# Kernel tuning notes

Measured on AMD Instinct MI355X. Metric: run time of the kernel, lower is better.

## Reference

```python
import jax, jax.numpy as jnp
import numpy as np

D = 1024
NUM_HEADS = 16
HEAD_DIM = D // NUM_HEADS
INIT_VALUES = 1e-4


def setup_inputs() -> dict:
    key = jax.random.key(0)
    ks = jax.random.split(key, 24)
    s = 0.02
    inp = {
        "v": jax.random.normal(ks[0], (8, 2048, D), dtype=jnp.float32),
        "l": jax.random.normal(ks[1], (8, 512, D), dtype=jnp.float32),
        "ln_v_g": jnp.ones((D,), jnp.float32),
        "ln_v_b": jnp.zeros((D,), jnp.float32),
        "ln_l_g": jnp.ones((D,), jnp.float32),
        "ln_l_b": jnp.zeros((D,), jnp.float32),
        "gamma_v": jnp.full((D,), INIT_VALUES, jnp.float32),
        "gamma_l": jnp.full((D,), INIT_VALUES, jnp.float32),
    }
    names = ["Wq_v2l", "Wk_v2l", "Wv_v2l", "Wo_v2l", "Wq_l2v", "Wk_l2v", "Wv_l2v", "Wo_l2v"]
    for i, n in enumerate(names):
        inp[n] = jax.random.normal(ks[2 + i], (D, D), dtype=jnp.float32) * s
        inp[n.replace("W", "b")] = jnp.zeros((D,), jnp.float32)
    return inp


def layer_norm(x, g, b, eps=1e-5):
    mu = jnp.mean(x, axis=-1, keepdims=True)
    var = jnp.var(x, axis=-1, keepdims=True)
    return (x - mu) * jax.lax.rsqrt(var + eps) * g + b


def mha(q_in, k_in, v_in, Wq, bq, Wk, bk, Wv, bv, Wo, bo):
    B, Sq, _ = q_in.shape
    Sk = k_in.shape[1]
    # torch Linear: x @ W.T + b
    q = (q_in @ Wq.T + bq).reshape(B, Sq, NUM_HEADS, HEAD_DIM)
    k = (k_in @ Wk.T + bk).reshape(B, Sk, NUM_HEADS, HEAD_DIM)
    v = (v_in @ Wv.T + bv).reshape(B, Sk, NUM_HEADS, HEAD_DIM)
    scores = jnp.einsum("bqhd,bkhd->bhqk", q, k) / np.sqrt(HEAD_DIM).astype(np.float32)
    attn = jax.nn.softmax(scores, axis=-1)
    ctx = jnp.einsum("bhqk,bkhd->bqhd", attn, v).reshape(B, Sq, D)
    return ctx @ Wo.T + bo


def reference(v, l, ln_v_g, ln_v_b, ln_l_g, ln_l_b, gamma_v, gamma_l,
              Wq_v2l, bq_v2l, Wk_v2l, bk_v2l, Wv_v2l, bv_v2l, Wo_v2l, bo_v2l,
              Wq_l2v, bq_l2v, Wk_l2v, bk_l2v, Wv_l2v, bv_l2v, Wo_l2v, bo_l2v):
    # eval mode: dropout and drop_path are identity
    v_norm = layer_norm(v, ln_v_g, ln_v_b)
    l_norm = layer_norm(l, ln_l_g, ln_l_b)
    updated_v = mha(v_norm, l_norm, l_norm,
                    Wq_v2l, bq_v2l, Wk_v2l, bk_v2l, Wv_v2l, bv_v2l, Wo_v2l, bo_v2l)
    updated_l = mha(l_norm, v_norm, v_norm,
                    Wq_l2v, bq_l2v, Wk_l2v, bk_l2v, Wv_l2v, bv_l2v, Wo_l2v, bo_l2v)
    v_out = v + gamma_v * updated_v
    l_out = l + gamma_l * updated_l
    return (v_out, l_out)
```

## Files before the change

kernel.cpp:

```cpp
#include <hip/hip_runtime.h>
#include <hip/hip_bf16.h>
#include <stdint.h>

typedef __bf16 bf16x8 __attribute__((ext_vector_type(8)));
typedef float f32x4 __attribute__((ext_vector_type(4)));
typedef float f32x16 __attribute__((ext_vector_type(16)));
typedef uint32_t u32x4 __attribute__((ext_vector_type(4)));
typedef unsigned short u16;

typedef __attribute__((address_space(1))) void as1_void;
typedef __attribute__((address_space(3))) void as3_void;

#define BAR() __builtin_amdgcn_s_barrier()
#define VMCNT(n) asm volatile("s_waitcnt vmcnt(" #n ")" ::: "memory")
#define LGKM0() asm volatile("s_waitcnt lgkmcnt(0)" ::: "memory")

__device__ __forceinline__ u16 f2bf(float f) {
  uint32_t u = __float_as_uint(f);
  u += 0x7fffu + ((u >> 16) & 1u);
  return (u16)(u >> 16);
}

struct Seg {
  const u16* W;
  const float* bias;
  u16* outb;
  float* outf;
  const float* res;
  const float* gamma;
  int mode;
  int sk;
  float ascale;
};

__global__ __launch_bounds__(256) void cvt8_kernel(
    const float4* s0, const float4* s1, const float4* s2, const float4* s3,
    const float4* s4, const float4* s5, const float4* s6, const float4* s7,
    ushort4* d0, ushort4* d1, ushort4* d2, ushort4* d3,
    ushort4* d4, ushort4* d5, ushort4* d6, ushort4* d7) {
  const float4* s; ushort4* d;
  switch (blockIdx.y) {
    case 0: s = s0; d = d0; break;
    case 1: s = s1; d = d1; break;
    case 2: s = s2; d = d2; break;
    case 3: s = s3; d = d3; break;
    case 4: s = s4; d = d4; break;
    case 5: s = s5; d = d5; break;
    case 6: s = s6; d = d6; break;
    default: s = s7; d = d7; break;
  }
  int i = blockIdx.x * 256 + threadIdx.x;
  float4 v = s[i];
  ushort4 o;
  o.x = f2bf(v.x); o.y = f2bf(v.y); o.z = f2bf(v.z); o.w = f2bf(v.w);
  d[i] = o;
}

__global__ __launch_bounds__(256) void ln_kernel(const float* __restrict__ x,
                                                 const float* __restrict__ g,
                                                 const float* __restrict__ b,
                                                 u16* __restrict__ out) {
  int row = blockIdx.x;
  int t = threadIdx.x;
  const float4* xr = (const float4*)(x + (size_t)row * 1024);
  float4 v = xr[t];
  float s = v.x + v.y + v.z + v.w;
  float s2 = v.x * v.x + v.y * v.y + v.z * v.z + v.w * v.w;
#pragma unroll
  for (int off = 1; off < 64; off <<= 1) {
    s += __shfl_xor(s, off);
    s2 += __shfl_xor(s2, off);
  }
  __shared__ float red[8];
  int wv = t >> 6;
  if ((t & 63) == 0) { red[wv] = s; red[4 + wv] = s2; }
  __syncthreads();
  s = red[0] + red[1] + red[2] + red[3];
  s2 = red[4] + red[5] + red[6] + red[7];
  float mu = s * (1.0f / 1024.0f);
  float var = s2 * (1.0f / 1024.0f) - mu * mu;
  float rstd = rsqrtf(var + 1e-5f);
  const float4 gv = ((const float4*)g)[t];
  const float4 bv = ((const float4*)b)[t];
  ushort4 o;
  o.x = f2bf((v.x - mu) * rstd * gv.x + bv.x);
  o.y = f2bf((v.y - mu) * rstd * gv.y + bv.y);
  o.z = f2bf((v.z - mu) * rstd * gv.z + bv.z);
  o.w = f2bf((v.w - mu) * rstd * gv.w + bv.w);
  ((ushort4*)out)[(size_t)row * 256 + t] = o;
}

__global__ __launch_bounds__(256, 3) void gemm_v8(
    const u16* __restrict__ A0, Seg s00, Seg s01, Seg s02, int mt0c, int nt0c,
    const u16* __restrict__ A1, Seg s10, Seg s11, Seg s12, int mt1c, int nt1c) {
  const int K = 1024;
  int bid = blockIdx.x;
  int nb0 = mt0c * nt0c;
  const u16* A;
  Seg sa, sb, sc;
  int mtiles, ntiles, lbid;
  if (bid < nb0) {
    A = A0; mtiles = mt0c; ntiles = nt0c; lbid = bid; sa = s00; sb = s01; sc = s02;
  } else {
    A = A1; mtiles = mt1c; ntiles = nt1c; lbid = bid - nb0; sa = s10; sb = s11; sc = s12;
  }
  int xcd = lbid & 7, q = lbid >> 3;
  int mchunk = mtiles >> 3;
  int mt = xcd * mchunk + q / ntiles;
  int nt = q % ntiles;
  int m0 = mt * 128;
  int si = nt >> 3;
  Seg seg = (si == 0) ? sa : (si == 1) ? sb : sc;
  int nl0 = (nt & 7) * 128;

  int t = threadIdx.x, lane = t & 63, wv = t >> 6;
  int wr = wv >> 1, wc = wv & 1;
  int lr = lane & 15, lg = lane >> 4;

  __shared__ u16 SA[3][128 * 32];
  __shared__ u16 SB[3][128 * 32];

  int row0 = t >> 2, c0 = t & 3;
  int sco = (c0 ^ ((row0 >> 1) & 3)) * 8;
  const u16* gA0 = A + (size_t)(m0 + row0) * K + sco;
  const u16* gB0 = seg.W + (size_t)(nl0 + row0) * K + sco;

  auto STAGE = [&](int slot, int kt) {
    __builtin_amdgcn_global_load_lds((const as1_void*)(gA0 + kt * 32),
                                     (as3_void*)(&SA[slot][0] + t * 8), 16, 0, 0);
    __builtin_amdgcn_global_load_lds((const as1_void*)(gA0 + (size_t)64 * K + kt * 32),
                                     (as3_void*)(&SA[slot][0] + 2048 + t * 8), 16, 0, 0);
    __builtin_amdgcn_global_load_lds((const as1_void*)(gB0 + kt * 32),
                                     (as3_void*)(&SB[slot][0] + t * 8), 16, 0, 0);
    __builtin_amdgcn_global_load_lds((const as1_void*)(gB0 + (size_t)64 * K + kt * 32),
                                     (as3_void*)(&SB[slot][0] + 2048 + t * 8), 16, 0, 0);
  };

  f32x4 acc[4][4] = {};

  STAGE(0, 0); STAGE(1, 1); STAGE(2, 2);
  VMCNT(8);
  BAR();

  int slot = 0;
  const int NKT = K / 32;
#pragma unroll 1
  for (int kt = 0; kt < NKT; ++kt) {
    bf16x8 aX[4], bX[4];
#pragma unroll
    for (int m = 0; m < 4; ++m) {
      int row = wr * 64 + m * 16 + lr;
      aX[m] = *(const bf16x8*)(&SA[slot][0] + row * 32 + ((lg ^ ((row >> 1) & 3)) * 8));
    }
#pragma unroll
    for (int n = 0; n < 4; ++n) {
      int row = wc * 64 + n * 16 + lr;
      bX[n] = *(const bf16x8*)(&SB[slot][0] + row * 32 + ((lg ^ ((row >> 1) & 3)) * 8));
    }
    __builtin_amdgcn_s_setprio(1);
#pragma unroll
    for (int m = 0; m < 4; ++m)
#pragma unroll
      for (int n = 0; n < 4; ++n)
        acc[m][n] = __builtin_amdgcn_mfma_f32_16x16x32_bf16(aX[m], bX[n], acc[m][n], 0, 0, 0);
    __builtin_amdgcn_s_setprio(0);
    LGKM0();
    if (kt + 2 < NKT) { VMCNT(4); }
    else if (kt + 1 < NKT) { VMCNT(0); }
    BAR();
    if (kt + 3 < NKT) STAGE(slot, kt + 3);
    slot = (slot == 2) ? 0 : slot + 1;
  }

  int rowb = m0 + wr * 64 + (lane >> 4) * 4;
#pragma unroll
  for (int m = 0; m < 4; ++m) {
#pragma unroll
    for (int n = 0; n < 4; ++n) {
      int scol = nl0 + wc * 64 + n * 16 + lr;
      float bcol = seg.bias[scol];
      int row = rowb + m * 16;
      if (seg.mode == 2) {
        int bb = row >> seg.sk;
        int ss = row & ((1 << seg.sk) - 1);
        int h = scol >> 6, d = scol & 63;
        ushort4 o;
        o.x = f2bf(acc[m][n][0] + bcol);
        o.y = f2bf(acc[m][n][1] + bcol);
        o.z = f2bf(acc[m][n][2] + bcol);
        o.w = f2bf(acc[m][n][3] + bcol);
        *(ushort4*)(seg.outb + ((((size_t)bb * 16 + h) * 64 + d) << seg.sk) + ss) = o;
      } else if (seg.mode == 0) {
#pragma unroll
        for (int r = 0; r < 4; ++r)
          seg.outb[(size_t)(row + r) * 1024 + scol] = f2bf((acc[m][n][r] + bcol) * seg.ascale);
      } else {
#pragma unroll
        for (int r = 0; r < 4; ++r) {
          size_t idx = (size_t)(row + r) * 1024 + scol;
          seg.outf[idx] = seg.res[idx] + seg.gamma[scol] * (acc[m][n][r] + bcol);
        }
      }
    }
  }
}

__global__ __launch_bounds__(256, 4) void attn2_kernel(
    const u16* __restrict__ Q0, const u16* __restrict__ K0,
    const u16* __restrict__ V0, u16* __restrict__ C0, int Sq0, int Sk0, int nqs0, int nb0,
    const u16* __restrict__ Q1, const u16* __restrict__ K1,
    const u16* __restrict__ V1, u16* __restrict__ C1, int Sq1, int Sk1, int nqs1) {
  int bid = blockIdx.x;
  const u16 *Q, *Kmat, *Vt;
  u16* ctx;
  int Sq, Sk, nq_shift, f;
  if (bid < nb0) {
    Q = Q0; Kmat = K0; Vt = V0; ctx = C0; Sq = Sq0; Sk = Sk0; nq_shift = nqs0; f = bid;
  } else {
    Q = Q1; Kmat = K1; Vt = V1; ctx = C1; Sq = Sq1; Sk = Sk1; nq_shift = nqs1; f = bid - nb0;
  }
  int xcd = f & 7, slot = f >> 3;
  int group = xcd * 16 + (slot >> nq_shift);
  int qt = slot & ((1 << nq_shift) - 1);
  int b = group >> 4, h = group & 15;
  int t = threadIdx.x, lane = t & 63, wv = t >> 6;
  int l31 = lane & 31, hi = lane >> 5;

  __shared__ u16 Ks[2][64 * 64];
  __shared__ u16 Vs[2][64 * 64];

  int q0 = qt * 128 + wv * 32;
  const u16* Qb = Q + (size_t)(b * Sq + q0 + l31) * 1024 + h * 64 + hi * 8;
  bf16x8 qf[4];
#pragma unroll
  for (int ds = 0; ds < 4; ++ds) qf[ds] = *(const bf16x8*)(Qb + ds * 16);

  int trow = t >> 3, tc = t & 7;
  int sc = (tc ^ (trow & 7)) * 8;
  const u16* gk = Kmat + (size_t)(b * Sk + trow) * 1024 + h * 64 + sc;
  const u16* gv = Vt + (size_t)((b * 16 + h) * 64 + trow) * Sk + sc;

  auto STAGE = [&](int buf, int kt) {
    const u16* k0 = gk + (size_t)(kt * 64) * 1024;
    const u16* v0 = gv + kt * 64;
    __builtin_amdgcn_global_load_lds((const as1_void*)k0, (as3_void*)(Ks[buf] + t * 8), 16, 0, 0);
    __builtin_amdgcn_global_load_lds((const as1_void*)(k0 + (size_t)32 * 1024), (as3_void*)(Ks[buf] + 2048 + t * 8), 16, 0, 0);
    __builtin_amdgcn_global_load_lds((const as1_void*)v0, (as3_void*)(Vs[buf] + t * 8), 16, 0, 0);
    __builtin_amdgcn_global_load_lds((const as1_void*)(v0 + (size_t)32 * Sk), (as3_void*)(Vs[buf] + 2048 + t * 8), 16, 0, 0);
  };

  STAGE(0, 0);
  __syncthreads();

  f32x16 acc0 = {}, acc1 = {};
  float m_run = -1e30f, l_run = 0.f;
  int sw = l31 & 7;

  int nt = Sk >> 6;
  for (int kt = 0; kt < nt; ++kt) {
    int cur = kt & 1;
    if (kt + 1 < nt) STAGE(cur ^ 1, kt + 1);
    const u16* kb = Ks[cur];
    f32x16 s0v = {}, s1v = {};
    __builtin_amdgcn_s_setprio(1);
#pragma unroll
    for (int ds = 0; ds < 4; ++ds) {
      int blk = 2 * ds + hi;
      bf16x8 ka0 = *(const bf16x8*)(kb + l31 * 64 + ((blk ^ sw) * 8));
      bf16x8 ka1 = *(const bf16x8*)(kb + (32 + l31) * 64 + ((blk ^ sw) * 8));
      s0v = __builtin_amdgcn_mfma_f32_32x32x16_bf16(ka0, qf[ds], s0v, 0, 0, 0);
      s1v = __builtin_amdgcn_mfma_f32_32x32x16_bf16(ka1, qf[ds], s1v, 0, 0, 0);
    }
    __builtin_amdgcn_s_setprio(0);
    float mx = s0v[0];
#pragma unroll
    for (int i = 1; i < 16; ++i) mx = fmaxf(mx, s0v[i]);
#pragma unroll
    for (int i = 0; i < 16; ++i) mx = fmaxf(mx, s1v[i]);
    mx = fmaxf(mx, __shfl_xor(mx, 32));
    if (__any(mx > m_run + 8.f)) {
      float mnew = fmaxf(m_run, mx);
      float fac = __builtin_amdgcn_exp2f(m_run - mnew);
#pragma unroll
      for (int r = 0; r < 16; ++r) {
        int src = (r & 3) + 8 * (r >> 2) + 4 * hi;
        float fr = __shfl(fac, src);
        acc0[r] *= fr;
        acc1[r] *= fr;
      }
      l_run *= fac;
      m_run = mnew;
    }
    float sum = 0.f;
#pragma unroll
    for (int i = 0; i < 16; ++i) {
      s0v[i] = __builtin_amdgcn_exp2f(s0v[i] - m_run);
      sum += s0v[i];
    }
#pragma unroll
    for (int i = 0; i < 16; ++i) {
      s1v[i] = __builtin_amdgcn_exp2f(s1v[i] - m_run);
      sum += s1v[i];
    }
    sum += __shfl_xor(sum, 32);
    l_run += sum;
    bf16x8 pa[4];
#pragma unroll
    for (int g = 0; g < 2; ++g) {
      const f32x16& s = g ? s1v : s0v;
#pragma unroll
      for (int half = 0; half < 2; ++half) {
        int o = half * 8;
        uint32_t a0, a1, b0, b1;
        asm("v_cvt_pk_bf16_f32 %0, %1, %2" : "=v"(a0) : "v"(s[o + 0]), "v"(s[o + 1]));
        asm("v_cvt_pk_bf16_f32 %0, %1, %2" : "=v"(a1) : "v"(s[o + 2]), "v"(s[o + 3]));
        asm("v_cvt_pk_bf16_f32 %0, %1, %2" : "=v"(b0) : "v"(s[o + 4]), "v"(s[o + 5]));
        asm("v_cvt_pk_bf16_f32 %0, %1, %2" : "=v"(b1) : "v"(s[o + 6]), "v"(s[o + 7]));
        asm("v_permlane32_swap_b32 %0, %1" : "+v"(a0), "+v"(b0));
        asm("v_permlane32_swap_b32 %0, %1" : "+v"(a1), "+v"(b1));
        u32x4 w;
        w[0] = a0; w[1] = a1; w[2] = b0; w[3] = b1;
        pa[g * 2 + half] = __builtin_bit_cast(bf16x8, w);
      }
    }
    const u16* vb = Vs[cur];
    __builtin_amdgcn_s_setprio(1);
#pragma unroll
    for (int ks = 0; ks < 4; ++ks) {
      int blk = 2 * ks + hi;
      bf16x8 vf0 = *(const bf16x8*)(vb + l31 * 64 + ((blk ^ sw) * 8));
      bf16x8 vf1 = *(const bf16x8*)(vb + (32 + l31) * 64 + ((blk ^ sw) * 8));
      acc0 = __builtin_amdgcn_mfma_f32_32x32x16_bf16(pa[ks], vf0, acc0, 0, 0, 0);
      acc1 = __builtin_amdgcn_mfma_f32_32x32x16_bf16(pa[ks], vf1, acc1, 0, 0, 0);
    }
    __builtin_amdgcn_s_setprio(0);
    __syncthreads();
  }
  float linv = 1.0f / l_run;
  u16* cb = ctx + (size_t)(b * Sq + q0) * 1024 + h * 64;
#pragma unroll
  for (int r = 0; r < 16; ++r) {
    int src = (r & 3) + 8 * (r >> 2) + 4 * hi;
    float li = __shfl(linv, src);
    cb[(size_t)src * 1024 + l31] = f2bf(acc0[r] * li);
    cb[(size_t)src * 1024 + 32 + l31] = f2bf(acc1[r] * li);
  }
}

extern "C" void kernel_launch(void* const* d_in, const int* in_sizes, int n_in,
                              void* d_out, int out_size, void* d_ws, size_t ws_size,
                              hipStream_t stream) {
  const float* v = (const float*)d_in[0];
  const float* l = (const float*)d_in[1];
  const float* ln_v_g = (const float*)d_in[2];
  const float* ln_v_b = (const float*)d_in[3];
  const float* ln_l_g = (const float*)d_in[4];
  const float* ln_l_b = (const float*)d_in[5];
  const float* gamma_v = (const float*)d_in[6];
  const float* gamma_l = (const float*)d_in[7];
  const float* Wf[8];
  const float* Bf[8];
  for (int i = 0; i < 8; ++i) {
    Wf[i] = (const float*)d_in[8 + 2 * i];
    Bf[i] = (const float*)d_in[9 + 2 * i];
  }
  float* v_out = (float*)d_out;
  float* l_out = v_out + (size_t)16384 * 1024;

  char* p = (char*)d_ws;
  auto alloc = [&](size_t bytes) {
    char* r = p;
    p += (bytes + 255) & ~(size_t)255;
    return r;
  };
  u16* Wbf[8];
  for (int i = 0; i < 8; ++i) Wbf[i] = (u16*)alloc((size_t)1024 * 1024 * 2);
  u16* vn   = (u16*)alloc((size_t)16384 * 1024 * 2);
  u16* lnm  = (u16*)alloc((size_t)4096 * 1024 * 2);
  u16* bufA = (u16*)alloc((size_t)16384 * 1024 * 2);
  u16* bufB = (u16*)alloc((size_t)4096 * 1024 * 2);
  u16* bufC = (u16*)alloc((size_t)4096 * 1024 * 2);
  u16* bufD = (u16*)alloc((size_t)16384 * 1024 * 2);
  u16* bufF = (u16*)alloc((size_t)4096 * 1024 * 2);
  u16* bufG = (u16*)alloc((size_t)16384 * 1024 * 2);

  const float QSC = 0.125f * 1.4426950408889634f;
  Seg zs = {};

  cvt8_kernel<<<dim3(1024, 8), 256, 0, stream>>>(
      (const float4*)Wf[0], (const float4*)Wf[1], (const float4*)Wf[2], (const float4*)Wf[3],
      (const float4*)Wf[4], (const float4*)Wf[5], (const float4*)Wf[6], (const float4*)Wf[7],
      (ushort4*)Wbf[0], (ushort4*)Wbf[1], (ushort4*)Wbf[2], (ushort4*)Wbf[3],
      (ushort4*)Wbf[4], (ushort4*)Wbf[5], (ushort4*)Wbf[6], (ushort4*)Wbf[7]);
  ln_kernel<<<16384, 256, 0, stream>>>(v, ln_v_g, ln_v_b, vn);
  ln_kernel<<<4096, 256, 0, stream>>>(l, ln_l_g, ln_l_b, lnm);

  {
    Seg a = {Wbf[4], Bf[4], bufB, nullptr, nullptr, nullptr, 0, 0, QSC};
    Seg b = {Wbf[1], Bf[1], bufF, nullptr, nullptr, nullptr, 0, 0, 1.0f};
    Seg c = {Wbf[2], Bf[2], bufC, nullptr, nullptr, nullptr, 2, 9, 1.0f};
    Seg q = {Wbf[0], Bf[0], bufA, nullptr, nullptr, nullptr, 0, 0, QSC};
    Seg k = {Wbf[5], Bf[5], bufG, nullptr, nullptr, nullptr, 0, 0, 1.0f};
    Seg vv = {Wbf[6], Bf[6], bufD, nullptr, nullptr, nullptr, 2, 11, 1.0f};
    gemm_v8<<<dim3(768 + 3072), 256, 0, stream>>>(lnm, a, b, c, 32, 24,
                                                  vn, q, k, vv, 128, 24);
  }
  attn2_kernel<<<dim3(2048 + 512), 256, 0, stream>>>(
      bufA, bufF, bufC, bufA, 2048, 512, 4, 2048,
      bufB, bufG, bufD, bufB, 512, 2048, 2);
  {
    Seg ov = {Wbf[3], Bf[3], nullptr, v_out, v, gamma_v, 1, 0, 1.0f};
    Seg ol = {Wbf[7], Bf[7], nullptr, l_out, l, gamma_l, 1, 0, 1.0f};
    gemm_v8<<<dim3(1024 + 256), 256, 0, stream>>>(bufA, ov, zs, zs, 128, 8,
                                                  bufB, ol, zs, zs, 32, 8);
  }
}
```

Measured before the change: 423.0 us.

## Enlarge GEMM tile to 256x128 per block and fuse weight cast with layernorms

The GEMM block tile grows from 128x128 to 256x128. Each wave now computes a 64x128 strip with 32 accumulators and reuses the shared B tile across all four waves, which halves the block count and the A/B reloads from global memory. Occupancy drops from 3 to 2 blocks per CU, and LDS and register use per block go up. Separately, the weight bf16 cast and both layernorms are merged into a single prep kernel, replacing three launches with one.

```diff
diff --git a/kernel.cpp b/kernel.cpp
--- a/kernel.cpp
+++ b/kernel.cpp
@@ -33,45 +33,53 @@
   float ascale;
 };
 
-__global__ __launch_bounds__(256) void cvt8_kernel(
-    const float4* s0, const float4* s1, const float4* s2, const float4* s3,
-    const float4* s4, const float4* s5, const float4* s6, const float4* s7,
-    ushort4* d0, ushort4* d1, ushort4* d2, ushort4* d3,
-    ushort4* d4, ushort4* d5, ushort4* d6, ushort4* d7) {
-  const float4* s; ushort4* d;
-  switch (blockIdx.y) {
-    case 0: s = s0; d = d0; break;
-    case 1: s = s1; d = d1; break;
-    case 2: s = s2; d = d2; break;
-    case 3: s = s3; d = d3; break;
-    case 4: s = s4; d = d4; break;
-    case 5: s = s5; d = d5; break;
-    case 6: s = s6; d = d6; break;
-    default: s = s7; d = d7; break;
-  }
-  int i = blockIdx.x * 256 + threadIdx.x;
-  float4 v = s[i];
-  ushort4 o;
-  o.x = f2bf(v.x); o.y = f2bf(v.y); o.z = f2bf(v.z); o.w = f2bf(v.w);
-  d[i] = o;
-}
-
-__global__ __launch_bounds__(256) void ln_kernel(const float* __restrict__ x,
-                                                 const float* __restrict__ g,
-                                                 const float* __restrict__ b,
-                                                 u16* __restrict__ out) {
-  int row = blockIdx.x;
-  int t = threadIdx.x;
+__global__ __launch_bounds__(256) void prep_kernel(
+    const float4* w0, const float4* w1, const float4* w2, const float4* w3,
+    const float4* w4, const float4* w5, const float4* w6, const float4* w7,
+    ushort4* o0, ushort4* o1, ushort4* o2, ushort4* o3,
+    ushort4* o4, ushort4* o5, ushort4* o6, ushort4* o7,
+    const float* v, const float* ln_v_g, const float* ln_v_b, u16* vn,
+    const float* l, const float* ln_l_g, const float* ln_l_b, u16* lnm) {
+  __shared__ float red[8];
+  int bid = blockIdx.x, t = threadIdx.x;
+  if (bid < 8192) {
+    int w = bid >> 10;
+    int i = ((bid & 1023) << 8) + t;
+    const float4* s;
+    ushort4* d;
+    switch (w) {
+      case 0: s = w0; d = o0; break;
+      case 1: s = w1; d = o1; break;
+      case 2: s = w2; d = o2; break;
+      case 3: s = w3; d = o3; break;
+      case 4: s = w4; d = o4; break;
+      case 5: s = w5; d = o5; break;
+      case 6: s = w6; d = o6; break;
+      default: s = w7; d = o7; break;
+    }
+    float4 x = s[i];
+    ushort4 o;
+    o.x = f2bf(x.x); o.y = f2bf(x.y); o.z = f2bf(x.z); o.w = f2bf(x.w);
+    d[i] = o;
+    return;
+  }
+  const float *x, *g, *b;
+  u16* out;
+  int row;
+  if (bid < 24576) {
+    x = v; g = ln_v_g; b = ln_v_b; out = vn; row = bid - 8192;
+  } else {
+    x = l; g = ln_l_g; b = ln_l_b; out = lnm; row = bid - 24576;
+  }
   const float4* xr = (const float4*)(x + (size_t)row * 1024);
-  float4 v = xr[t];
-  float s = v.x + v.y + v.z + v.w;
-  float s2 = v.x * v.x + v.y * v.y + v.z * v.z + v.w * v.w;
+  float4 vv = xr[t];
+  float s = vv.x + vv.y + vv.z + vv.w;
+  float s2 = vv.x * vv.x + vv.y * vv.y + vv.z * vv.z + vv.w * vv.w;
 #pragma unroll
   for (int off = 1; off < 64; off <<= 1) {
     s += __shfl_xor(s, off);
     s2 += __shfl_xor(s2, off);
   }
-  __shared__ float red[8];
   int wv = t >> 6;
   if ((t & 63) == 0) { red[wv] = s; red[4 + wv] = s2; }
   __syncthreads();
@@ -83,14 +91,14 @@
   const float4 gv = ((const float4*)g)[t];
   const float4 bv = ((const float4*)b)[t];
   ushort4 o;
-  o.x = f2bf((v.x - mu) * rstd * gv.x + bv.x);
-  o.y = f2bf((v.y - mu) * rstd * gv.y + bv.y);
-  o.z = f2bf((v.z - mu) * rstd * gv.z + bv.z);
-  o.w = f2bf((v.w - mu) * rstd * gv.w + bv.w);
+  o.x = f2bf((vv.x - mu) * rstd * gv.x + bv.x);
+  o.y = f2bf((vv.y - mu) * rstd * gv.y + bv.y);
+  o.z = f2bf((vv.z - mu) * rstd * gv.z + bv.z);
+  o.w = f2bf((vv.w - mu) * rstd * gv.w + bv.w);
   ((ushort4*)out)[(size_t)row * 256 + t] = o;
 }
 
-__global__ __launch_bounds__(256, 3) void gemm_v8(
+__global__ __launch_bounds__(256, 2) void gemm_v9(
     const u16* __restrict__ A0, Seg s00, Seg s01, Seg s02, int mt0c, int nt0c,
     const u16* __restrict__ A1, Seg s10, Seg s11, Seg s12, int mt1c, int nt1c) {
   const int K = 1024;
@@ -108,16 +116,15 @@
   int mchunk = mtiles >> 3;
   int mt = xcd * mchunk + q / ntiles;
   int nt = q % ntiles;
-  int m0 = mt * 128;
+  int m0 = mt * 256;
   int si = nt >> 3;
   Seg seg = (si == 0) ? sa : (si == 1) ? sb : sc;
   int nl0 = (nt & 7) * 128;
 
   int t = threadIdx.x, lane = t & 63, wv = t >> 6;
-  int wr = wv >> 1, wc = wv & 1;
   int lr = lane & 15, lg = lane >> 4;
 
-  __shared__ u16 SA[3][128 * 32];
+  __shared__ u16 SA[3][256 * 32];
   __shared__ u16 SB[3][128 * 32];
 
   int row0 = t >> 2, c0 = t & 3;
@@ -126,58 +133,60 @@
   const u16* gB0 = seg.W + (size_t)(nl0 + row0) * K + sco;
 
   auto STAGE = [&](int slot, int kt) {
-    __builtin_amdgcn_global_load_lds((const as1_void*)(gA0 + kt * 32),
-                                     (as3_void*)(&SA[slot][0] + t * 8), 16, 0, 0);
-    __builtin_amdgcn_global_load_lds((const as1_void*)(gA0 + (size_t)64 * K + kt * 32),
-                                     (as3_void*)(&SA[slot][0] + 2048 + t * 8), 16, 0, 0);
-    __builtin_amdgcn_global_load_lds((const as1_void*)(gB0 + kt * 32),
-                                     (as3_void*)(&SB[slot][0] + t * 8), 16, 0, 0);
-    __builtin_amdgcn_global_load_lds((const as1_void*)(gB0 + (size_t)64 * K + kt * 32),
-                                     (as3_void*)(&SB[slot][0] + 2048 + t * 8), 16, 0, 0);
+#pragma unroll
+    for (int h = 0; h < 4; ++h)
+      __builtin_amdgcn_global_load_lds(
+          (const as1_void*)(gA0 + (size_t)(h * 64) * K + kt * 32),
+          (as3_void*)(&SA[slot][0] + h * 2048 + t * 8), 16, 0, 0);
+#pragma unroll
+    for (int h = 0; h < 2; ++h)
+      __builtin_amdgcn_global_load_lds(
+          (const as1_void*)(gB0 + (size_t)(h * 64) * K + kt * 32),
+          (as3_void*)(&SB[slot][0] + h * 2048 + t * 8), 16, 0, 0);
   };
 
-  f32x4 acc[4][4] = {};
+  f32x4 acc[4][8] = {};
 
   STAGE(0, 0); STAGE(1, 1); STAGE(2, 2);
-  VMCNT(8);
+  VMCNT(12);
   BAR();
 
   int slot = 0;
   const int NKT = K / 32;
 #pragma unroll 1
   for (int kt = 0; kt < NKT; ++kt) {
-    bf16x8 aX[4], bX[4];
+    bf16x8 aX[4], bX[8];
 #pragma unroll
     for (int m = 0; m < 4; ++m) {
-      int row = wr * 64 + m * 16 + lr;
+      int row = wv * 64 + m * 16 + lr;
       aX[m] = *(const bf16x8*)(&SA[slot][0] + row * 32 + ((lg ^ ((row >> 1) & 3)) * 8));
     }
 #pragma unroll
-    for (int n = 0; n < 4; ++n) {
-      int row = wc * 64 + n * 16 + lr;
+    for (int n = 0; n < 8; ++n) {
+      int row = n * 16 + lr;
       bX[n] = *(const bf16x8*)(&SB[slot][0] + row * 32 + ((lg ^ ((row >> 1) & 3)) * 8));
     }
     __builtin_amdgcn_s_setprio(1);
 #pragma unroll
     for (int m = 0; m < 4; ++m)
 #pragma unroll
-      for (int n = 0; n < 4; ++n)
+      for (int n = 0; n < 8; ++n)
         acc[m][n] = __builtin_amdgcn_mfma_f32_16x16x32_bf16(aX[m], bX[n], acc[m][n], 0, 0, 0);
     __builtin_amdgcn_s_setprio(0);
     LGKM0();
-    if (kt + 2 < NKT) { VMCNT(4); }
+    if (kt + 2 < NKT) { VMCNT(6); }
     else if (kt + 1 < NKT) { VMCNT(0); }
     BAR();
     if (kt + 3 < NKT) STAGE(slot, kt + 3);
     slot = (slot == 2) ? 0 : slot + 1;
   }
 
-  int rowb = m0 + wr * 64 + (lane >> 4) * 4;
+  int rowb = m0 + wv * 64 + lg * 4;
 #pragma unroll
   for (int m = 0; m < 4; ++m) {
 #pragma unroll
-    for (int n = 0; n < 4; ++n) {
-      int scol = nl0 + wc * 64 + n * 16 + lr;
+    for (int n = 0; n < 8; ++n) {
+      int scol = nl0 + n * 16 + lr;
       float bcol = seg.bias[scol];
       int row = rowb + m * 16;
       if (seg.mode == 2) {
@@ -387,13 +396,12 @@
   const float QSC = 0.125f * 1.4426950408889634f;
   Seg zs = {};
 
-  cvt8_kernel<<<dim3(1024, 8), 256, 0, stream>>>(
+  prep_kernel<<<dim3(28672), 256, 0, stream>>>(
       (const float4*)Wf[0], (const float4*)Wf[1], (const float4*)Wf[2], (const float4*)Wf[3],
       (const float4*)Wf[4], (const float4*)Wf[5], (const float4*)Wf[6], (const float4*)Wf[7],
       (ushort4*)Wbf[0], (ushort4*)Wbf[1], (ushort4*)Wbf[2], (ushort4*)Wbf[3],
-      (ushort4*)Wbf[4], (ushort4*)Wbf[5], (ushort4*)Wbf[6], (ushort4*)Wbf[7]);
-  ln_kernel<<<16384, 256, 0, stream>>>(v, ln_v_g, ln_v_b, vn);
-  ln_kernel<<<4096, 256, 0, stream>>>(l, ln_l_g, ln_l_b, lnm);
+      (ushort4*)Wbf[4], (ushort4*)Wbf[5], (ushort4*)Wbf[6], (ushort4*)Wbf[7],
+      v, ln_v_g, ln_v_b, vn, l, ln_l_g, ln_l_b, lnm);
 
   {
     Seg a = {Wbf[4], Bf[4], bufB, nullptr, nullptr, nullptr, 0, 0, QSC};
@@ -402,8 +410,8 @@
     Seg q = {Wbf[0], Bf[0], bufA, nullptr, nullptr, nullptr, 0, 0, QSC};
     Seg k = {Wbf[5], Bf[5], bufG, nullptr, nullptr, nullptr, 0, 0, 1.0f};
     Seg vv = {Wbf[6], Bf[6], bufD, nullptr, nullptr, nullptr, 2, 11, 1.0f};
-    gemm_v8<<<dim3(768 + 3072), 256, 0, stream>>>(lnm, a, b, c, 32, 24,
-                                                  vn, q, k, vv, 128, 24);
+    gemm_v9<<<dim3(16 * 24 + 64 * 24), 256, 0, stream>>>(lnm, a, b, c, 16, 24,
+                                                         vn, q, k, vv, 64, 24);
   }
   attn2_kernel<<<dim3(2048 + 512), 256, 0, stream>>>(
       bufA, bufF, bufC, bufA, 2048, 512, 4, 2048,
@@ -411,7 +419,7 @@
   {
     Seg ov = {Wbf[3], Bf[3], nullptr, v_out, v, gamma_v, 1, 0, 1.0f};
     Seg ol = {Wbf[7], Bf[7], nullptr, l_out, l, gamma_l, 1, 0, 1.0f};
-    gemm_v8<<<dim3(1024 + 256), 256, 0, stream>>>(bufA, ov, zs, zs, 128, 8,
-                                                  bufB, ol, zs, zs, 32, 8);
+    gemm_v9<<<dim3(64 * 8 + 16 * 8), 256, 0, stream>>>(bufA, ov, zs, zs, 64, 8,
+                                                       bufB, ol, zs, zs, 16, 8);
   }
 }
```

Result: slower. 467.1 us (+10.4%).
